# Performance work log

Hardware: AMD Instinct MI355X
Metric: run time of the kernel (lower is better)

The kernel has to match this reference:

```python
import jax, jax.numpy as jnp
import numpy as np

N, E, F_NODE, F_EDGE, H, L, G = 4096, 12288, 64, 16, 128, 4, 256
BN_EPS = 1e-5


def setup_inputs() -> dict:
    key = jax.random.key(0)
    ks = jax.random.split(key, 20)
    s = lambda k, shape, fan: jax.random.normal(k, shape, jnp.float32) * (1.0 / np.sqrt(fan))
    inp = {
        'x': jax.random.normal(ks[0], (N, F_NODE), jnp.float32),
        'edge_index': jax.random.randint(ks[1], (2, E), 0, N, dtype=jnp.int64),
        'edge_attr': jax.random.normal(ks[2], (E, F_EDGE), jnp.float32),
        'batch': jnp.sort(jax.random.randint(ks[3], (N,), 0, G, dtype=jnp.int64)),
        # node encoder
        'node_w': s(ks[4], (F_NODE, H), F_NODE),
        'node_b': jnp.zeros((H,), jnp.float32),
        # per-layer edge MLP: edge_feat -> 128 -> H*H
        'e1_w': s(ks[5], (L, F_EDGE, 128), F_EDGE),
        'e1_b': jnp.zeros((L, 128), jnp.float32),
        'e2_w': s(ks[6], (L, 128, H * H), 128) * 0.1,
        'e2_b': jnp.zeros((L, H * H), jnp.float32),
        # NNConv root weight + bias
        'root_w': s(ks[7], (L, H, H), H),
        'conv_b': jnp.zeros((L, H), jnp.float32),
        # batchnorm affine
        'bn_g': jnp.ones((L, H), jnp.float32),
        'bn_b': jnp.zeros((L, H), jnp.float32),
        # head
        'head_w1': s(ks[8], (H, H), H),
        'head_b1': jnp.zeros((H,), jnp.float32),
        'head_w2': s(ks[9], (H, 1), H),
        'head_b2': jnp.zeros((1,), jnp.float32),
    }
    return inp


def reference(x, edge_index, edge_attr, batch, node_w, node_b, e1_w, e1_b,
              e2_w, e2_b, root_w, conv_b, bn_g, bn_b, head_w1, head_b1,
              head_w2, head_b2):
    src, dst = edge_index[0], edge_index[1]
    h = x @ node_w + node_b  # [N,H]
    # in-degree for mean aggregation
    deg = jax.ops.segment_sum(jnp.ones((E,), h.dtype), dst, num_segments=N)
    inv_deg = jnp.where(deg > 0, 1.0 / jnp.maximum(deg, 1.0), 0.0)[:, None]
    for l in range(L):
        # edge MLP -> per-edge [H,H] weight
        e = jax.nn.relu(edge_attr @ e1_w[l] + e1_b[l])            # [E,128]
        W_e = (e @ e2_w[l] + e2_b[l]).reshape(E, H, H)            # [E,H,H]
        msg = jnp.einsum('eh,eho->eo', h[src], W_e)               # [E,H]
        agg = jax.ops.segment_sum(msg, dst, num_segments=N) * inv_deg
        out = agg + h @ root_w[l] + conv_b[l]
        # batchnorm (training-mode batch stats, biased var as in torch)
        mu = out.mean(0)
        var = out.var(0)
        out = (out - mu) * jax.lax.rsqrt(var + BN_EPS) * bn_g[l] + bn_b[l]
        h = h + jax.nn.relu(out)  # dropout disabled (eval)
    # global mean pool over graphs
    cnt = jax.ops.segment_sum(jnp.ones((N,), h.dtype), batch, num_segments=G)
    pooled = jax.ops.segment_sum(h, batch, num_segments=G) / jnp.maximum(cnt, 1.0)[:, None]
    y = jax.nn.relu(pooled @ head_w1 + head_b1) @ head_w2 + head_b2
    return y.squeeze(-1)  # [G]
```

## Files before the change

kernel.cpp:

```cpp
#include <hip/hip_runtime.h>

#define N_NODES 4096
#define E_TOT   12288
#define F_NODE  64
#define F_EDGE  16
#define HDIM    128
#define NLAYER  4
#define NGRAPH  256

typedef _Float16 half8 __attribute__((ext_vector_type(8)));
typedef float    f32x4 __attribute__((ext_vector_type(4)));

__global__ __launch_bounds__(256)
void k_prep_w2(const float* __restrict__ e2w, const float* __restrict__ e2b,
               _Float16* __restrict__ W2F)
{
    __shared__ _Float16 pg[16384];
    int b = blockIdx.x;
    int l = b / 129, k = b - l * 129;
    const float* src = (k < 128) ? (e2w + ((size_t)(l * 128 + k)) * 16384)
                                 : (e2b + (size_t)l * 16384);
    int t = threadIdx.x;
#pragma unroll
    for (int it = 0; it < 16; ++it) {
        int p = it * 1024 + t * 4;
        float4 v = *(const float4*)(src + p);
#pragma unroll
        for (int j4 = 0; j4 < 4; ++j4) {
            int p_ = p + j4;
            int h  = p_ >> 7, o = p_ & 127;
            int idx = ((h >> 5) * 8 + (o >> 4)) * 512
                    + (((h >> 3) & 3) * 16 + (o & 15)) * 8 + (h & 7);
            float val = (j4 == 0) ? v.x : (j4 == 1) ? v.y : (j4 == 2) ? v.z : v.w;
            pg[idx] = (_Float16)val;
        }
    }
    __syncthreads();
    _Float16* dst = W2F + (size_t)b * 16384;
#pragma unroll
    for (int it = 0; it < 8; ++it) {
        int i = it * 2048 + t * 8;
        *(half8*)(dst + i) = *(const half8*)(pg + i);
    }
}

__global__ __launch_bounds__(128)
void k_node_enc(const float* __restrict__ x, const float* __restrict__ nw,
                const float* __restrict__ nb, float* __restrict__ h,
                _Float16* __restrict__ hf)
{
    __shared__ float xl[F_NODE];
    int n = blockIdx.x, o = threadIdx.x;
    if (o < F_NODE) xl[o] = x[(size_t)n * F_NODE + o];
    __syncthreads();
    float acc = nb[o];
#pragma unroll 8
    for (int f = 0; f < F_NODE; ++f) acc += xl[f] * nw[f * HDIM + o];
    h [(size_t)n * HDIM + o] = acc;
    hf[(size_t)n * HDIM + o] = (_Float16)acc;
}

__global__ void k_deg(const int* __restrict__ dst, int* __restrict__ deg)
{
    int e = blockIdx.x * 256 + threadIdx.x;
    if (e < E_TOT) atomicAdd(&deg[dst[e]], 1);
}

__global__ void k_invd(const int* __restrict__ deg, float* __restrict__ invd)
{
    int n = blockIdx.x * 256 + threadIdx.x;
    if (n < N_NODES) invd[n] = deg[n] > 0 ? 1.0f / (float)deg[n] : 0.0f;
}

#define BM 64
#define KSPLIT 4
__global__ __launch_bounds__(256, 3)
void k_msg(const _Float16* __restrict__ W2L,
           const float* __restrict__ ea,
           const float* __restrict__ w1,
           const float* __restrict__ b1,
           const _Float16* __restrict__ hf,
           const int* __restrict__ srcIdx,
           const int* __restrict__ dstIdx,
           float* __restrict__ agg,
           float* __restrict__ bns1,
           float* __restrict__ bns2)
{
    __shared__ float    al[BM][17];
    __shared__ _Float16 efs[BM][40];

    const int tid  = threadIdx.x;
    const int lane = tid & 63;
    const int w    = tid >> 6;
    const int lhi  = lane >> 4;
    const int llo  = lane & 15;

    const int bx    = blockIdx.x;
    const int ks    = (bx & 7) >> 1;
    const int tile  = (bx >> 3) * 2 + (bx & 1);
    const int e0    = tile * BM;
    const int kbase = (129 * ks) >> 2;
    const int kcnt  = ((129 * (ks + 1)) >> 2) - kbase;

    if (bx == 0 && tid < HDIM) { bns1[tid] = 0.f; bns2[tid] = 0.f; }

    {
        int e = tid >> 2, f0 = (tid & 3) * 4;
        const float* p = ea + (size_t)(e0 + e) * F_EDGE + f0;
        al[e][f0 + 0] = p[0];
        al[e][f0 + 1] = p[1];
        al[e][f0 + 2] = p[2];
        al[e][f0 + 3] = p[3];
    }

    half8 hs[4][4];
#pragma unroll
    for (int rf = 0; rf < 4; ++rf) {
        int s = srcIdx[e0 + rf * 16 + llo];
        const _Float16* hp = hf + (size_t)s * HDIM + lhi * 8;
#pragma unroll
        for (int hc = 0; hc < 4; ++hc)
            hs[rf][hc] = *(const half8*)(hp + hc * 32);
    }

    __syncthreads();

    {
        int e = tid >> 2, q = tid & 3;
        int c0 = q * 9;
        int c1 = c0 + 9 < kcnt ? c0 + 9 : kcnt;
        for (int c = c0; c < c1; ++c) {
            int kg = kbase + c;
            float a;
            if (kg == 128) {
                a = 1.0f;
            } else {
                a = b1[kg];
#pragma unroll
                for (int f = 0; f < F_EDGE; ++f) a += al[e][f] * w1[f * HDIM + kg];
                a = fmaxf(a, 0.f);
            }
            efs[e][c] = (_Float16)a;
        }
    }

    __syncthreads();

    const _Float16* bp = W2L + (size_t)kbase * 16384 + (w * 2) * 512 + lane * 8;

#define LDQ(d0, d1, kk, hc) do {                                            \
        const _Float16* p_ = bp + (size_t)(kk) * 16384 + (hc) * 4096;       \
        d0 = *(const half8*)(p_); d1 = *(const half8*)(p_ + 512);           \
    } while (0)

    half8 b00, b01, b10, b11, b20, b21, b30, b31;
    LDQ(b00, b01, 0, 0);
    LDQ(b10, b11, 0, 1);
    LDQ(b20, b21, 0, 2);
    LDQ(b30, b31, 0, 3);

    f32x4 acc[4][2];
#pragma unroll
    for (int rf = 0; rf < 4; ++rf)
#pragma unroll
        for (int cf = 0; cf < 2; ++cf)
#pragma unroll
            for (int d = 0; d < 4; ++d) acc[rf][cf][d] = 0.f;

    for (int kk = 0; kk < kcnt; ++kk) {
        const bool nx = (kk + 1 < kcnt);
        _Float16 efv[4];
#pragma unroll
        for (int rf = 0; rf < 4; ++rf) efv[rf] = efs[rf * 16 + llo][kk];

#pragma unroll
        for (int rf = 0; rf < 4; ++rf) {
            half8 av = hs[rf][0] * efv[rf];
            acc[rf][0] = __builtin_amdgcn_mfma_f32_16x16x32_f16(av, b00, acc[rf][0], 0, 0, 0);
            acc[rf][1] = __builtin_amdgcn_mfma_f32_16x16x32_f16(av, b01, acc[rf][1], 0, 0, 0);
        }
        if (nx) LDQ(b00, b01, kk + 1, 0);

#pragma unroll
        for (int rf = 0; rf < 4; ++rf) {
            half8 av = hs[rf][1] * efv[rf];
            acc[rf][0] = __builtin_amdgcn_mfma_f32_16x16x32_f16(av, b10, acc[rf][0], 0, 0, 0);
            acc[rf][1] = __builtin_amdgcn_mfma_f32_16x16x32_f16(av, b11, acc[rf][1], 0, 0, 0);
        }
        if (nx) LDQ(b10, b11, kk + 1, 1);

#pragma unroll
        for (int rf = 0; rf < 4; ++rf) {
            half8 av = hs[rf][2] * efv[rf];
            acc[rf][0] = __builtin_amdgcn_mfma_f32_16x16x32_f16(av, b20, acc[rf][0], 0, 0, 0);
            acc[rf][1] = __builtin_amdgcn_mfma_f32_16x16x32_f16(av, b21, acc[rf][1], 0, 0, 0);
        }
        if (nx) LDQ(b20, b21, kk + 1, 2);

#pragma unroll
        for (int rf = 0; rf < 4; ++rf) {
            half8 av = hs[rf][3] * efv[rf];
            acc[rf][0] = __builtin_amdgcn_mfma_f32_16x16x32_f16(av, b30, acc[rf][0], 0, 0, 0);
            acc[rf][1] = __builtin_amdgcn_mfma_f32_16x16x32_f16(av, b31, acc[rf][1], 0, 0, 0);
        }
        if (nx) LDQ(b30, b31, kk + 1, 3);
    }
#undef LDQ

#pragma unroll
    for (int rf = 0; rf < 4; ++rf) {
#pragma unroll
        for (int r = 0; r < 4; ++r) {
            int row = rf * 16 + lhi * 4 + r;
            int d   = dstIdx[e0 + row];
#pragma unroll
            for (int cf = 0; cf < 2; ++cf) {
                int o = w * 32 + cf * 16 + llo;
                atomicAdd(&agg[(size_t)d * HDIM + o], acc[rf][cf][r]);
            }
        }
    }
}

__global__ __launch_bounds__(128)
void k_out(const float* __restrict__ agg, const float* __restrict__ invd,
           const float* __restrict__ h, const float* __restrict__ rw,
           const float* __restrict__ cb, float* __restrict__ outb,
           float* __restrict__ bns1, float* __restrict__ bns2)
{
    __shared__ float hl[16][132];
    __shared__ float rb1[128], rb2[128];
    int t = threadIdx.x, n0 = blockIdx.x * 16;
    int rg = t >> 5, cg = t & 31;
    for (int i = t; i < 16 * HDIM; i += 128)
        hl[i >> 7][i & 127] = h[(size_t)(n0 + (i >> 7)) * HDIM + (i & 127)];
    rb1[t] = 0.f; rb2[t] = 0.f;
    __syncthreads();

    f32x4 cbv = *(const f32x4*)&cb[cg * 4];
    f32x4 acc[4];
#pragma unroll
    for (int i = 0; i < 4; ++i) {
        int r = n0 + rg * 4 + i;
        f32x4 a = *(const f32x4*)&agg[(size_t)r * HDIM + cg * 4];
        acc[i] = a * invd[r] + cbv;
    }
    for (int hh = 0; hh < HDIM; hh += 4) {
        f32x4 wv[4], hv[4];
#pragma unroll
        for (int j = 0; j < 4; ++j) wv[j] = *(const f32x4*)&rw[(hh + j) * HDIM + cg * 4];
#pragma unroll
        for (int i = 0; i < 4; ++i) hv[i] = *(const f32x4*)&hl[rg * 4 + i][hh];
#pragma unroll
        for (int i = 0; i < 4; ++i)
#pragma unroll
            for (int j = 0; j < 4; ++j)
                acc[i] += hv[i][j] * wv[j];
    }
    f32x4 s1v = {0.f,0.f,0.f,0.f}, s2v = {0.f,0.f,0.f,0.f};
#pragma unroll
    for (int i = 0; i < 4; ++i) {
        *(f32x4*)&outb[(size_t)(n0 + rg * 4 + i) * HDIM + cg * 4] = acc[i];
        s1v += acc[i];
        s2v += acc[i] * acc[i];
    }
#pragma unroll
    for (int j = 0; j < 4; ++j) {
        atomicAdd(&rb1[cg * 4 + j], s1v[j]);
        atomicAdd(&rb2[cg * 4 + j], s2v[j]);
    }
    __syncthreads();
    atomicAdd(&bns1[t], rb1[t]);
    atomicAdd(&bns2[t], rb2[t]);
}

__global__ void k_bn_apply(const float* __restrict__ outb, const float* __restrict__ bns1,
                           const float* __restrict__ bns2, const float* __restrict__ g,
                           const float* __restrict__ b, float* __restrict__ h,
                           _Float16* __restrict__ hf, float* __restrict__ agg,
                           const int* __restrict__ batch, float* __restrict__ pooled,
                           int* __restrict__ cnt, int last)
{
    int i = blockIdx.x * 256 + threadIdx.x;
    int o = i & (HDIM - 1);
    const float inv_n = 1.0f / (float)N_NODES;
    float m   = bns1[o] * inv_n;
    float var = bns2[o] * inv_n - m * m;
    float rs  = rsqrtf(var + 1e-5f);
    float v  = (outb[i] - m) * rs * g[o] + b[o];
    float hn = h[i] + fmaxf(v, 0.f);
    h[i]  = hn;
    hf[i] = (_Float16)hn;
    if (!last) {
        agg[i] = 0.f;
    } else {
        int n  = i >> 7;
        int gg = batch[n];
        atomicAdd(&pooled[(size_t)gg * HDIM + o], hn);
        if (o == 0) atomicAdd(&cnt[gg], 1);
    }
}

__global__ __launch_bounds__(128)
void k_head(const float* __restrict__ pooled, const int* __restrict__ cnt,
            const float* __restrict__ w1, const float* __restrict__ b1,
            const float* __restrict__ w2, const float* __restrict__ b2,
            float* __restrict__ y)
{
    __shared__ float pl[HDIM];
    __shared__ float red[HDIM];
    int g = blockIdx.x, o = threadIdx.x;
    float ic = 1.0f / (float)max(cnt[g], 1);
    pl[o] = pooled[(size_t)g * HDIM + o] * ic;
    __syncthreads();
    float t = b1[o];
#pragma unroll 8
    for (int hh = 0; hh < HDIM; ++hh) t += pl[hh] * w1[hh * HDIM + o];
    t = fmaxf(t, 0.f);
    red[o] = t * w2[o];
    __syncthreads();
    for (int s = 64; s > 0; s >>= 1) {
        if (o < s) red[o] += red[o + s];
        __syncthreads();
    }
    if (o == 0) y[g] = red[0] + b2[0];
}

extern "C" void kernel_launch(void* const* d_in, const int* in_sizes, int n_in,
                              void* d_out, int out_size, void* d_ws, size_t ws_size,
                              hipStream_t stream)
{
    const float* x      = (const float*)d_in[0];
    const int*   ei     = (const int*)  d_in[1];
    const float* ea     = (const float*)d_in[2];
    const int*   batch  = (const int*)  d_in[3];
    const float* node_w = (const float*)d_in[4];
    const float* node_b = (const float*)d_in[5];
    const float* e1w    = (const float*)d_in[6];
    const float* e1b    = (const float*)d_in[7];
    const float* e2w    = (const float*)d_in[8];
    const float* e2b    = (const float*)d_in[9];
    const float* rw     = (const float*)d_in[10];
    const float* cb     = (const float*)d_in[11];
    const float* bng    = (const float*)d_in[12];
    const float* bnb    = (const float*)d_in[13];
    const float* hw1    = (const float*)d_in[14];
    const float* hb1    = (const float*)d_in[15];
    const float* hw2    = (const float*)d_in[16];
    const float* hb2    = (const float*)d_in[17];
    float* y = (float*)d_out;

    char* ws = (char*)d_ws;
    _Float16* W2F  = (_Float16*)ws; ws += 16908288;
    float*    h    = (float*)ws;    ws += 2097152;
    _Float16* hf   = (_Float16*)ws; ws += 1048576;
    float*    agg  = (float*)ws;    ws += 2097152;
    float*    bns1 = (float*)ws;    ws += 512;
    float*    bns2 = (float*)ws;    ws += 512;
    float*    outb = (float*)ws;    ws += 2097152;
    int*      deg  = (int*)ws;      ws += 16384;
    float*    invd = (float*)ws;    ws += 16384;
    float*    pooled = (float*)ws;  ws += 131072;
    int*      cnt  = (int*)ws;      ws += 1024;

    const int* src = ei;
    const int* dst = ei + E_TOT;

    k_prep_w2<<<NLAYER * 129, 256, 0, stream>>>(e2w, e2b, W2F);
    k_node_enc<<<N_NODES, 128, 0, stream>>>(x, node_w, node_b, h, hf);
    hipMemsetAsync(deg, 0, N_NODES * sizeof(int), stream);
    k_deg<<<(E_TOT + 255) / 256, 256, 0, stream>>>(dst, deg);
    k_invd<<<(N_NODES + 255) / 256, 256, 0, stream>>>(deg, invd);
    hipMemsetAsync(agg, 0, (size_t)N_NODES * HDIM * sizeof(float), stream);
    hipMemsetAsync(pooled, 0, (size_t)NGRAPH * HDIM * sizeof(float) + NGRAPH * sizeof(int), stream);

    for (int l = 0; l < NLAYER; ++l) {
        k_msg<<<(E_TOT / BM) * KSPLIT, 256, 0, stream>>>(
            W2F + (size_t)l * 129 * 16384, ea,
            e1w + l * F_EDGE * HDIM, e1b + l * HDIM,
            hf, src, dst, agg, bns1, bns2);
        k_out<<<N_NODES / 16, 128, 0, stream>>>(agg, invd, h,
                                                rw + l * HDIM * HDIM,
                                                cb + l * HDIM, outb, bns1, bns2);
        k_bn_apply<<<(N_NODES * HDIM) / 256, 256, 0, stream>>>(
            outb, bns1, bns2, bng + l * HDIM, bnb + l * HDIM, h, hf,
            agg, batch, pooled, cnt, (l == NLAYER - 1) ? 1 : 0);
    }

    k_head<<<NGRAPH, 128, 0, stream>>>(pooled, cnt, hw1, hb1, hw2, hb2, y);
}
```

Measured before the change: 431.6 us.

## Precompute edge MLP activations in separate kernel and regroup W2 prefetch

Moves the first edge-MLP layer (relu(ea@w1+b1) plus the bias-one column) out of the message kernel into a dedicated per-layer kernel that writes fp16 activations to a padded global buffer. The message kernel now just copies its k-slice into shared memory with vector loads, removing scalar global w1 reads and one barrier. The W2 fragment prefetch is regrouped into two half-batches per k step. This adds one launch per layer and an extra global round trip for the activations.

```diff
diff --git a/kernel.cpp b/kernel.cpp
--- a/kernel.cpp
+++ b/kernel.cpp
@@ -72,13 +72,41 @@
     if (n < N_NODES) invd[n] = deg[n] > 0 ? 1.0f / (float)deg[n] : 0.0f;
 }
 
+#define EF_STRIDE 136
+__global__ __launch_bounds__(256)
+void k_edge_mlp(const float* __restrict__ ea, const float* __restrict__ w1,
+                const float* __restrict__ b1, _Float16* __restrict__ efg)
+{
+    __shared__ float al[16][17];
+    __shared__ float wl[16][HDIM];
+    __shared__ float bl[HDIM];
+    int t = threadIdx.x, e0 = blockIdx.x * 16;
+    if (t < HDIM) bl[t] = b1[t];
+    for (int i = t; i < F_EDGE * HDIM; i += 256) wl[i >> 7][i & 127] = w1[i];
+    { int i = t; al[i >> 4][i & 15] = ea[(size_t)e0 * F_EDGE + i]; }
+    __syncthreads();
+    int e = t >> 4, og = t & 15;
+    float acc[8];
+#pragma unroll
+    for (int j = 0; j < 8; ++j) acc[j] = bl[og * 8 + j];
+#pragma unroll
+    for (int f = 0; f < F_EDGE; ++f) {
+        float a = al[e][f];
+#pragma unroll
+        for (int j = 0; j < 8; ++j) acc[j] += a * wl[f][og * 8 + j];
+    }
+    half8 o;
+#pragma unroll
+    for (int j = 0; j < 8; ++j) o[j] = (_Float16)fmaxf(acc[j], 0.f);
+    *(half8*)&efg[(size_t)(e0 + e) * EF_STRIDE + og * 8] = o;
+    if (og == 0) efg[(size_t)(e0 + e) * EF_STRIDE + 128] = (_Float16)1.0f;
+}
+
 #define BM 64
 #define KSPLIT 4
 __global__ __launch_bounds__(256, 3)
 void k_msg(const _Float16* __restrict__ W2L,
-           const float* __restrict__ ea,
-           const float* __restrict__ w1,
-           const float* __restrict__ b1,
+           const _Float16* __restrict__ efg,
            const _Float16* __restrict__ hf,
            const int* __restrict__ srcIdx,
            const int* __restrict__ dstIdx,
@@ -86,7 +114,6 @@
            float* __restrict__ bns1,
            float* __restrict__ bns2)
 {
-    __shared__ float    al[BM][17];
     __shared__ _Float16 efs[BM][40];
 
     const int tid  = threadIdx.x;
@@ -104,13 +131,10 @@
 
     if (bx == 0 && tid < HDIM) { bns1[tid] = 0.f; bns2[tid] = 0.f; }
 
-    {
-        int e = tid >> 2, f0 = (tid & 3) * 4;
-        const float* p = ea + (size_t)(e0 + e) * F_EDGE + f0;
-        al[e][f0 + 0] = p[0];
-        al[e][f0 + 1] = p[1];
-        al[e][f0 + 2] = p[2];
-        al[e][f0 + 3] = p[3];
+    for (int i = tid; i < BM * 5; i += 256) {
+        int r = i / 5, c = i - r * 5;
+        *(half8*)&efs[r][c * 8] =
+            *(const half8*)(efg + (size_t)(e0 + r) * EF_STRIDE + kbase + c * 8);
     }
 
     half8 hs[4][4];
@@ -125,87 +149,56 @@
 
     __syncthreads();
 
-    {
-        int e = tid >> 2, q = tid & 3;
-        int c0 = q * 9;
-        int c1 = c0 + 9 < kcnt ? c0 + 9 : kcnt;
-        for (int c = c0; c < c1; ++c) {
-            int kg = kbase + c;
-            float a;
-            if (kg == 128) {
-                a = 1.0f;
-            } else {
-                a = b1[kg];
-#pragma unroll
-                for (int f = 0; f < F_EDGE; ++f) a += al[e][f] * w1[f * HDIM + kg];
-                a = fmaxf(a, 0.f);
-            }
-            efs[e][c] = (_Float16)a;
+    const _Float16* bp = W2L + (size_t)kbase * 16384 + (w * 2) * 512 + lane * 8;
+
+#define LDH(dst, kk, h2) do {                                          \
+        const _Float16* p_ = bp + (size_t)(kk) * 16384 + (h2) * 8192;  \
+        dst[0] = *(const half8*)(p_);                                  \
+        dst[1] = *(const half8*)(p_ + 512);                            \
+        dst[2] = *(const half8*)(p_ + 4096);                           \
+        dst[3] = *(const half8*)(p_ + 4608);                           \
+    } while (0)
+
+    half8 B0[4], B1[4];
+    LDH(B0, 0, 0);
+    LDH(B1, 0, 1);
+
+    f32x4 acc[4][2];
+#pragma unroll
+    for (int rf = 0; rf < 4; ++rf)
+#pragma unroll
+        for (int cf = 0; cf < 2; ++cf)
+#pragma unroll
+            for (int d = 0; d < 4; ++d) acc[rf][cf][d] = 0.f;
+
+    for (int kk = 0; kk < kcnt; ++kk) {
+        _Float16 efv[4];
+#pragma unroll
+        for (int rf = 0; rf < 4; ++rf) efv[rf] = efs[rf * 16 + llo][kk];
+
+#pragma unroll
+        for (int rf = 0; rf < 4; ++rf) {
+            half8 av0 = hs[rf][0] * efv[rf];
+            half8 av1 = hs[rf][1] * efv[rf];
+            acc[rf][0] = __builtin_amdgcn_mfma_f32_16x16x32_f16(av0, B0[0], acc[rf][0], 0, 0, 0);
+            acc[rf][1] = __builtin_amdgcn_mfma_f32_16x16x32_f16(av0, B0[1], acc[rf][1], 0, 0, 0);
+            acc[rf][0] = __builtin_amdgcn_mfma_f32_16x16x32_f16(av1, B0[2], acc[rf][0], 0, 0, 0);
+            acc[rf][1] = __builtin_amdgcn_mfma_f32_16x16x32_f16(av1, B0[3], acc[rf][1], 0, 0, 0);
         }
-    }
-
-    __syncthreads();
-
-    const _Float16* bp = W2L + (size_t)kbase * 16384 + (w * 2) * 512 + lane * 8;
-
-#define LDQ(d0, d1, kk, hc) do {                                            \
-        const _Float16* p_ = bp + (size_t)(kk) * 16384 + (hc) * 4096;       \
-        d0 = *(const half8*)(p_); d1 = *(const half8*)(p_ + 512);           \
-    } while (0)
-
-    half8 b00, b01, b10, b11, b20, b21, b30, b31;
-    LDQ(b00, b01, 0, 0);
-    LDQ(b10, b11, 0, 1);
-    LDQ(b20, b21, 0, 2);
-    LDQ(b30, b31, 0, 3);
-
-    f32x4 acc[4][2];
-#pragma unroll
-    for (int rf = 0; rf < 4; ++rf)
-#pragma unroll
-        for (int cf = 0; cf < 2; ++cf)
-#pragma unroll
-            for (int d = 0; d < 4; ++d) acc[rf][cf][d] = 0.f;
-
-    for (int kk = 0; kk < kcnt; ++kk) {
-        const bool nx = (kk + 1 < kcnt);
-        _Float16 efv[4];
-#pragma unroll
-        for (int rf = 0; rf < 4; ++rf) efv[rf] = efs[rf * 16 + llo][kk];
+        if (kk + 1 < kcnt) LDH(B0, kk + 1, 0);
 
 #pragma unroll
         for (int rf = 0; rf < 4; ++rf) {
-            half8 av = hs[rf][0] * efv[rf];
-            acc[rf][0] = __builtin_amdgcn_mfma_f32_16x16x32_f16(av, b00, acc[rf][0], 0, 0, 0);
-            acc[rf][1] = __builtin_amdgcn_mfma_f32_16x16x32_f16(av, b01, acc[rf][1], 0, 0, 0);
+            half8 av2 = hs[rf][2] * efv[rf];
+            half8 av3 = hs[rf][3] * efv[rf];
+            acc[rf][0] = __builtin_amdgcn_mfma_f32_16x16x32_f16(av2, B1[0], acc[rf][0], 0, 0, 0);
+            acc[rf][1] = __builtin_amdgcn_mfma_f32_16x16x32_f16(av2, B1[1], acc[rf][1], 0, 0, 0);
+            acc[rf][0] = __builtin_amdgcn_mfma_f32_16x16x32_f16(av3, B1[2], acc[rf][0], 0, 0, 0);
+            acc[rf][1] = __builtin_amdgcn_mfma_f32_16x16x32_f16(av3, B1[3], acc[rf][1], 0, 0, 0);
         }
-        if (nx) LDQ(b00, b01, kk + 1, 0);
-
-#pragma unroll
-        for (int rf = 0; rf < 4; ++rf) {
-            half8 av = hs[rf][1] * efv[rf];
-            acc[rf][0] = __builtin_amdgcn_mfma_f32_16x16x32_f16(av, b10, acc[rf][0], 0, 0, 0);
-            acc[rf][1] = __builtin_amdgcn_mfma_f32_16x16x32_f16(av, b11, acc[rf][1], 0, 0, 0);
-        }
-        if (nx) LDQ(b10, b11, kk + 1, 1);
-
-#pragma unroll
-        for (int rf = 0; rf < 4; ++rf) {
-            half8 av = hs[rf][2] * efv[rf];
-            acc[rf][0] = __builtin_amdgcn_mfma_f32_16x16x32_f16(av, b20, acc[rf][0], 0, 0, 0);
-            acc[rf][1] = __builtin_amdgcn_mfma_f32_16x16x32_f16(av, b21, acc[rf][1], 0, 0, 0);
-        }
-        if (nx) LDQ(b20, b21, kk + 1, 2);
-
-#pragma unroll
-        for (int rf = 0; rf < 4; ++rf) {
-            half8 av = hs[rf][3] * efv[rf];
-            acc[rf][0] = __builtin_amdgcn_mfma_f32_16x16x32_f16(av, b30, acc[rf][0], 0, 0, 0);
-            acc[rf][1] = __builtin_amdgcn_mfma_f32_16x16x32_f16(av, b31, acc[rf][1], 0, 0, 0);
-        }
-        if (nx) LDQ(b30, b31, kk + 1, 3);
-    }
-#undef LDQ
+        if (kk + 1 < kcnt) LDH(B1, kk + 1, 1);
+    }
+#undef LDH
 
 #pragma unroll
     for (int rf = 0; rf < 4; ++rf) {
@@ -354,6 +347,7 @@
     _Float16* W2F  = (_Float16*)ws; ws += 16908288;
     float*    h    = (float*)ws;    ws += 2097152;
     _Float16* hf   = (_Float16*)ws; ws += 1048576;
+    _Float16* efg  = (_Float16*)ws; ws += 3342336;
     float*    agg  = (float*)ws;    ws += 2097152;
     float*    bns1 = (float*)ws;    ws += 512;
     float*    bns2 = (float*)ws;    ws += 512;
@@ -375,10 +369,10 @@
     hipMemsetAsync(pooled, 0, (size_t)NGRAPH * HDIM * sizeof(float) + NGRAPH * sizeof(int), stream);
 
     for (int l = 0; l < NLAYER; ++l) {
+        k_edge_mlp<<<E_TOT / 16, 256, 0, stream>>>(ea, e1w + l * F_EDGE * HDIM,
+                                                   e1b + l * HDIM, efg);
         k_msg<<<(E_TOT / BM) * KSPLIT, 256, 0, stream>>>(
-            W2F + (size_t)l * 129 * 16384, ea,
-            e1w + l * F_EDGE * HDIM, e1b + l * HDIM,
-            hf, src, dst, agg, bns1, bns2);
+            W2F + (size_t)l * 129 * 16384, efg, hf, src, dst, agg, bns1, bns2);
         k_out<<<N_NODES / 16, 128, 0, stream>>>(agg, invd, h,
                                                 rw + l * HDIM * HDIM,
                                                 cb + l * HDIM, outb, bns1, bns2);
```

Result: faster. 413.7 us, median of 2 (-4.2%).
